# Kernel tuning notes

Hardware: AMD Instinct MI355X
Metric: run time of the kernel (lower is better)

The kernel has to match this reference:

```python
import jax, jax.numpy as jnp
import numpy as np

NUM_CODES = 4096
EMBED_DIM = 256
N_TOKENS = 65536
COMMITMENT_COST = 0.1


def setup_inputs() -> dict:
    key = jax.random.key(0)
    k1, k2 = jax.random.split(key)
    z_e = jax.random.normal(k1, (N_TOKENS, EMBED_DIM), dtype=jnp.float32)
    embeddings = jax.random.normal(k2, (NUM_CODES, EMBED_DIM), dtype=jnp.float32)
    return {"z_e": z_e, "embeddings": embeddings}


def reference(z_e, embeddings):
    # Squared Euclidean distances (argmin-equivalent to torch.cdist):
    # d2[n,k] = |z_n|^2 - 2 z_n.E_k + |E_k|^2
    z_sq = jnp.sum(z_e * z_e, axis=-1, keepdims=True)          # [N,1]
    e_sq = jnp.sum(embeddings * embeddings, axis=-1)            # [K]
    d2 = z_sq - 2.0 * (z_e @ embeddings.T) + e_sq[None, :]      # [N,K]
    indices = jnp.argmin(d2, axis=-1)                           # [N] int

    z_q = embeddings[indices]                                   # [N,D] gather

    # commitment loss: mse(detach(z_q), z_e)
    diff = jax.lax.stop_gradient(z_q) - z_e
    commitment_loss = COMMITMENT_COST * jnp.mean(diff * diff)

    # straight-through estimator
    z_q_st = z_e + jax.lax.stop_gradient(z_q - z_e)

    # perplexity from code usage histogram (avoids materializing one-hot)
    counts = jnp.zeros((NUM_CODES,), dtype=jnp.float32).at[indices].add(1.0)
    avg_probs = counts / z_e.shape[0]
    perplexity = jnp.exp(-jnp.sum(avg_probs * jnp.log(avg_probs + 1e-10)))

    return z_q_st, indices, commitment_loss, perplexity
```

## Files before the change

kernel.cpp:

```cpp
#include <hip/hip_runtime.h>

#define N_TOKENS   65536
#define NUM_CODES  4096
#define EMBED_DIM  256

#define IDX_OFF  ((size_t)N_TOKENS * EMBED_DIM)
#define LOSS_OFF (IDX_OFF + N_TOKENS)

#define DELTA 0.2f
#define UCAP  16384
#define RT    8

typedef _Float16 half8 __attribute__((ext_vector_type(8)));
typedef float    f32x4 __attribute__((ext_vector_type(4)));
typedef unsigned long long u64;

__device__ __forceinline__ void gl_lds16(const void* g, void* l) {
    __builtin_amdgcn_global_load_lds(
        (const __attribute__((address_space(1))) unsigned int*)g,
        (__attribute__((address_space(3))) unsigned int*)l, 16, 0, 0);
}

__global__ void k_convE(const float* __restrict__ E, _Float16* __restrict__ Eh) {
    int gid = blockIdx.x * 256 + threadIdx.x;
    int n  = gid >> 5;
    int kg = gid & 31;
    const float* src = E + (size_t)n * EMBED_DIM + kg * 8;
    float4 a = *(const float4*)src;
    float4 b = *(const float4*)(src + 4);
    int ct = n >> 4, l15 = n & 15, kc = kg >> 2, q = kg & 3;
    int lane = q * 16 + l15;
    half8 hv;
    hv[0]=(_Float16)a.x; hv[1]=(_Float16)a.y; hv[2]=(_Float16)a.z; hv[3]=(_Float16)a.w;
    hv[4]=(_Float16)b.x; hv[5]=(_Float16)b.y; hv[6]=(_Float16)b.z; hv[7]=(_Float16)b.w;
    *(half8*)(Eh + ((size_t)(ct * 8 + kc) * 64 + lane) * 8) = hv;
}

__global__ void k_esq(const float* __restrict__ E, float* __restrict__ esq) {
    int k = blockIdx.x;
    int l = threadIdx.x;
    float4 v = *(const float4*)(E + (size_t)k * EMBED_DIM + l * 4);
    float s = v.x * v.x + v.y * v.y + v.z * v.z + v.w * v.w;
    #pragma unroll
    for (int off = 32; off; off >>= 1) s += __shfl_down(s, off, 64);
    if (l == 0) esq[k] = s;
}

__global__ void k_transpose(const float* __restrict__ E, float* __restrict__ Et) {
    __shared__ float t[32][33];
    int tx = threadIdx.x & 31, ty = threadIdx.x >> 5;
    int c0 = blockIdx.x * 32, d0 = blockIdx.y * 32;
    #pragma unroll
    for (int i = 0; i < 4; ++i)
        t[ty + 8 * i][tx] = E[(size_t)(c0 + ty + 8 * i) * EMBED_DIM + d0 + tx];
    __syncthreads();
    #pragma unroll
    for (int i = 0; i < 4; ++i)
        Et[(size_t)(d0 + ty + 8 * i) * NUM_CODES + c0 + tx] = t[tx][ty + 8 * i];
}

__launch_bounds__(256, 2)
__global__ void k_argmin_mfma(const float* __restrict__ Z, const _Float16* __restrict__ Eh,
                              const float* __restrict__ esq, int* __restrict__ out_idx,
                              int* __restrict__ ulist, int* __restrict__ ucount) {
    __shared__ __align__(16) _Float16 Bs[16384];
    __shared__ float esq_s[NUM_CODES];

    const int tid  = threadIdx.x;
    const int lane = tid & 63;
    const int w    = tid >> 6;
    const int w0   = w >> 1;
    const int w1   = w & 1;
    const int l15  = lane & 15;
    const int q    = lane >> 4;
    const int tb   = blockIdx.x;

    for (int i = tid; i < NUM_CODES; i += 256) esq_s[i] = esq[i];

    half8 A[4][8];
    const float* Zb = Z + ((size_t)tb * 128 + w0 * 64) * EMBED_DIM;
    #pragma unroll
    for (int rt = 0; rt < 4; ++rt) {
        const float* Zr = Zb + (rt * 16 + l15) * EMBED_DIM + q * 8;
        #pragma unroll
        for (int kc = 0; kc < 8; ++kc) {
            float4 a = *(const float4*)(Zr + kc * 32);
            float4 b = *(const float4*)(Zr + kc * 32 + 4);
            half8 hv;
            hv[0]=(_Float16)a.x; hv[1]=(_Float16)a.y; hv[2]=(_Float16)a.z; hv[3]=(_Float16)a.w;
            hv[4]=(_Float16)b.x; hv[5]=(_Float16)b.y; hv[6]=(_Float16)b.z; hv[7]=(_Float16)b.w;
            A[rt][kc] = hv;
        }
    }

    float best[16], sec[16];
    int   bidx[16];
    #pragma unroll
    for (int k = 0; k < 16; ++k) { best[k] = 1e30f; sec[k] = 1e30f; bidx[k] = 0; }

    const int cb = w1 * 2;

    for (int it = 0; it < NUM_CODES / 64; ++it) {
        __syncthreads();
        const _Float16* src = Eh + (size_t)it * 16384 + (w * 8) * 512 + lane * 8;
        #pragma unroll
        for (int s = 0; s < 8; ++s)
            gl_lds16(src + s * 512, Bs + (w * 8 + s) * 512);
        __syncthreads();

        f32x4 acc[4][2];
        #pragma unroll
        for (int rt = 0; rt < 4; ++rt) { acc[rt][0] = (f32x4)0.0f; acc[rt][1] = (f32x4)0.0f; }

        #pragma unroll
        for (int kc = 0; kc < 8; ++kc) {
            half8 bf0 = *(const half8*)(Bs + ((cb + 0) * 8 + kc) * 512 + lane * 8);
            half8 bf1 = *(const half8*)(Bs + ((cb + 1) * 8 + kc) * 512 + lane * 8);
            #pragma unroll
            for (int rt = 0; rt < 4; ++rt) {
                acc[rt][0] = __builtin_amdgcn_mfma_f32_16x16x32_f16(A[rt][kc], bf0, acc[rt][0], 0, 0, 0);
                acc[rt][1] = __builtin_amdgcn_mfma_f32_16x16x32_f16(A[rt][kc], bf1, acc[rt][1], 0, 0, 0);
            }
        }

        int code0 = it * 64 + cb * 16 + l15;
        #pragma unroll
        for (int c = 0; c < 2; ++c) {
            float e  = esq_s[code0 + c * 16];
            int code = code0 + c * 16;
            #pragma unroll
            for (int rt = 0; rt < 4; ++rt)
                #pragma unroll
                for (int r = 0; r < 4; ++r) {
                    float v = fmaf(-2.0f, acc[rt][c][r], e);
                    int k = rt * 4 + r;
                    float ob = best[k];
                    bool t = v < ob;
                    best[k] = t ? v : ob;
                    sec[k]  = fminf(sec[k], t ? ob : v);
                    bidx[k] = t ? code : bidx[k];
                }
        }
    }

    #pragma unroll
    for (int m = 1; m <= 8; m <<= 1) {
        #pragma unroll
        for (int k = 0; k < 16; ++k) {
            float ob = __shfl_xor(best[k], m, 64);
            float os = __shfl_xor(sec[k],  m, 64);
            int   oi = __shfl_xor(bidx[k], m, 64);
            float ns = fminf(fminf(sec[k], os), fmaxf(best[k], ob));
            bool t = (ob < best[k]) || (ob == best[k] && oi < bidx[k]);
            best[k] = t ? ob : best[k];
            bidx[k] = t ? oi : bidx[k];
            sec[k]  = ns;
        }
    }

    __syncthreads();
    float* mb = (float*)Bs;
    float* ms = mb + 256;
    int*   mi = (int*)(mb + 512);
    if (l15 == 0) {
        #pragma unroll
        for (int k = 0; k < 16; ++k) {
            int row = w0 * 64 + (k >> 2) * 16 + q * 4 + (k & 3);
            mb[row * 2 + w1] = best[k];
            ms[row * 2 + w1] = sec[k];
            mi[row * 2 + w1] = bidx[k];
        }
    }
    __syncthreads();
    if (tid < 128) {
        float b0 = mb[tid * 2], b1 = mb[tid * 2 + 1];
        float s0 = ms[tid * 2], s1 = ms[tid * 2 + 1];
        int   i0 = mi[tid * 2], i1 = mi[tid * 2 + 1];
        bool t = (b1 < b0) || (b1 == b0 && i1 < i0);
        float bb = t ? b1 : b0;
        int   ii = t ? i1 : i0;
        float ss = fminf(fminf(s0, s1), fmaxf(b0, b1));
        int token = tb * 128 + tid;
        out_idx[token] = ii;
        if (ss - bb < DELTA) {
            int p = atomicAdd(ucount, 1);
            if (p < UCAP) ulist[p] = token;
        }
    }
}

__launch_bounds__(256)
__global__ void k_refine(const float* __restrict__ Z, const float* __restrict__ Et,
                         const float* __restrict__ esq, const int* __restrict__ ulist,
                         const int* __restrict__ ucount, u64* __restrict__ umin) {
    int cnt = *ucount; if (cnt > UCAP) cnt = UCAP;
    const int g   = blockIdx.x >> 2;
    const int qtr = blockIdx.x & 3;
    if (g * RT >= cnt) return;

    __shared__ float zs[RT][256];
    const int tid  = threadIdx.x;
    const int lane = tid & 63;

    #pragma unroll
    for (int t = 0; t < RT; ++t) {
        int u = g * RT + t;
        int tok = ulist[(u < cnt) ? u : g * RT];
        zs[t][tid] = Z[(size_t)tok * EMBED_DIM + tid];
    }
    __syncthreads();

    const int c0 = qtr * 1024 + tid * 4;
    f32x4 acc[RT];
    #pragma unroll
    for (int t = 0; t < RT; ++t) acc[t] = (f32x4)0.0f;

    for (int d4 = 0; d4 < 64; ++d4) {
        f32x4 e0 = *(const f32x4*)(Et + (size_t)(d4 * 4 + 0) * NUM_CODES + c0);
        f32x4 e1 = *(const f32x4*)(Et + (size_t)(d4 * 4 + 1) * NUM_CODES + c0);
        f32x4 e2 = *(const f32x4*)(Et + (size_t)(d4 * 4 + 2) * NUM_CODES + c0);
        f32x4 e3 = *(const f32x4*)(Et + (size_t)(d4 * 4 + 3) * NUM_CODES + c0);
        #pragma unroll
        for (int t = 0; t < RT; ++t) {
            f32x4 z4 = *(const f32x4*)&zs[t][d4 * 4];
            acc[t] += z4.x * e0;
            acc[t] += z4.y * e1;
            acc[t] += z4.z * e2;
            acc[t] += z4.w * e3;
        }
    }

    f32x4 eq = *(const f32x4*)(esq + c0);
    #pragma unroll
    for (int t = 0; t < RT; ++t) {
        u64 p = ~0ull;
        #pragma unroll
        for (int r = 0; r < 4; ++r) {
            float v = fmaf(-2.0f, acc[t][r], eq[r]) + 4096.0f;
            u64 cand = ((u64)__float_as_uint(v) << 32) | (unsigned)(c0 + r);
            p = cand < p ? cand : p;
        }
        #pragma unroll
        for (int m = 1; m <= 32; m <<= 1) {
            u64 o = __shfl_xor(p, m, 64);
            p = o < p ? o : p;
        }
        int u = g * RT + t;
        if (lane == 0 && u < cnt) atomicMin(umin + u, p);
    }
}

__global__ void k_rwrite(const int* __restrict__ ulist, const int* __restrict__ ucount,
                         const u64* __restrict__ umin, int* __restrict__ out_idx) {
    int cnt = *ucount; if (cnt > UCAP) cnt = UCAP;
    int u = blockIdx.x * 256 + threadIdx.x;
    if (u < cnt) out_idx[ulist[u]] = (int)(umin[u] & 0xFFFFFFFFu);
}

__global__ void k_gather(const float* __restrict__ Z, const float* __restrict__ E,
                         float* __restrict__ out,
                         float* __restrict__ loss_parts, unsigned* __restrict__ hist) {
    int wave = threadIdx.x >> 6, lane = threadIdx.x & 63;
    int token = blockIdx.x * 4 + wave;
    int* idxi = (int*)(out + IDX_OFF);
    int k = idxi[token];
    float4 z = *(const float4*)(Z + (size_t)token * EMBED_DIM + lane * 4);
    float4 qv = *(const float4*)(E + (size_t)k * EMBED_DIM + lane * 4);
    *(float4*)(out + (size_t)token * EMBED_DIM + lane * 4) = qv;
    float dx = qv.x - z.x, dy = qv.y - z.y, dz = qv.z - z.z, dw = qv.w - z.w;
    float s = dx * dx + dy * dy + dz * dz + dw * dw;
    #pragma unroll
    for (int off = 32; off; off >>= 1) s += __shfl_down(s, off, 64);
    if (lane == 0) {
        atomicAdd(loss_parts + (blockIdx.x & 1023), s);
        atomicAdd(hist + k, 1u);
        out[IDX_OFF + token] = (float)k;
    }
}

__global__ void k_final(const float* __restrict__ loss_parts,
                        const unsigned* __restrict__ hist, float* __restrict__ out) {
    __shared__ float red[256];
    int t = threadIdx.x;
    float s = 0.0f;
    for (int i = t; i < 1024; i += 256) s += loss_parts[i];
    red[t] = s;
    __syncthreads();
    #pragma unroll
    for (int off = 128; off; off >>= 1) {
        if (t < off) red[t] += red[t + off];
        __syncthreads();
    }
    float loss = 0.1f * red[0] / (float)(N_TOKENS * EMBED_DIM);

    float h = 0.0f;
    for (int i = t; i < NUM_CODES; i += 256) {
        float p = (float)hist[i] / (float)N_TOKENS;
        h += p * logf(p + 1e-10f);
    }
    __syncthreads();
    red[t] = h;
    __syncthreads();
    #pragma unroll
    for (int off = 128; off; off >>= 1) {
        if (t < off) red[t] += red[t + off];
        __syncthreads();
    }
    if (t == 0) {
        out[LOSS_OFF]     = loss;
        out[LOSS_OFF + 1] = expf(-red[0]);
    }
}

extern "C" void kernel_launch(void* const* d_in, const int* in_sizes, int n_in,
                              void* d_out, int out_size, void* d_ws, size_t ws_size,
                              hipStream_t stream) {
    const float* Z = (const float*)d_in[0];
    const float* E = (const float*)d_in[1];
    float* out = (float*)d_out;
    char*  ob  = (char*)d_out;
    char*  ws  = (char*)d_ws;

    _Float16* Eh   = (_Float16*)(ob + 50331648);
    float*    Et   = (float*)(ob + 54525952);
    u64*      umin = (u64*)(ob + 58720256);
    int*      idx  = (int*)(out + IDX_OFF);

    float*    esq        = (float*)ws;
    int*      ulist      = (int*)(ws + 16384);
    int*      ucount     = (int*)(ws + 81920);
    float*    loss_parts = (float*)(ws + 81984);
    unsigned* hist       = (unsigned*)(ws + 86080);

    hipMemsetAsync(ws + 81920, 0, 64 + 4096 + 16384, stream);
    hipMemsetAsync(umin, 0xFF, (size_t)UCAP * 8, stream);

    k_convE      <<<(NUM_CODES * 32) / 256, 256, 0, stream>>>(E, Eh);
    k_esq        <<<NUM_CODES, 64, 0, stream>>>(E, esq);
    k_transpose  <<<dim3(NUM_CODES / 32, EMBED_DIM / 32), 256, 0, stream>>>(E, Et);
    k_argmin_mfma<<<N_TOKENS / 128, 256, 0, stream>>>(Z, Eh, esq, idx, ulist, ucount);
    k_refine     <<<4 * (UCAP / RT), 256, 0, stream>>>(Z, Et, esq, ulist, ucount, umin);
    k_rwrite     <<<UCAP / 256, 256, 0, stream>>>(ulist, ucount, umin, idx);
    k_gather     <<<N_TOKENS / 4, 256, 0, stream>>>(Z, E, out, loss_parts, hist);
    k_final      <<<1, 256, 0, stream>>>(loss_parts, hist, out);
}
```

Baseline: 342.8 us.

## Double-buffer codebook LDS tiles and pair-reduce distances before the running argmin

The shared codebook tile becomes two buffers, so the async global-to-LDS copy of the next 64-code tile is issued before the MFMA work on the current tile. This hides load latency behind compute and cuts the barriers per tile from two to one. The argmin update now compares the two candidate codes per row with each other first, then merges the winner into the running best and second-best, which saves a compare chain per element. The trade-off is double the LDS for the tile, which at two blocks per CU leaves very little headroom and may hurt occupancy.

New measurement: 354.0 us. +3.3%, slower.

```diff
diff --git a/kernel.cpp b/kernel.cpp
--- a/kernel.cpp
+++ b/kernel.cpp
@@ -63,7 +63,7 @@
 __global__ void k_argmin_mfma(const float* __restrict__ Z, const _Float16* __restrict__ Eh,
                               const float* __restrict__ esq, int* __restrict__ out_idx,
                               int* __restrict__ ulist, int* __restrict__ ucount) {
-    __shared__ __align__(16) _Float16 Bs[16384];
+    __shared__ __align__(16) _Float16 Bs[2][16384];
     __shared__ float esq_s[NUM_CODES];
 
     const int tid  = threadIdx.x;
@@ -74,6 +74,16 @@
     const int l15  = lane & 15;
     const int q    = lane >> 4;
     const int tb   = blockIdx.x;
+    const int cb   = w1 * 2;
+
+#define STAGE(itn, nb) do {                                                        \
+        const _Float16* _src = Eh + (size_t)(itn) * 16384 + (w * 8) * 512 + lane * 8; \
+        _Pragma("unroll")                                                          \
+        for (int s = 0; s < 8; ++s)                                                \
+            gl_lds16(_src + s * 512, &Bs[nb][(w * 8 + s) * 512]);                  \
+    } while (0)
+
+    STAGE(0, 0);
 
     for (int i = tid; i < NUM_CODES; i += 256) esq_s[i] = esq[i];
 
@@ -98,50 +108,56 @@
     #pragma unroll
     for (int k = 0; k < 16; ++k) { best[k] = 1e30f; sec[k] = 1e30f; bidx[k] = 0; }
 
-    const int cb = w1 * 2;
-
-    for (int it = 0; it < NUM_CODES / 64; ++it) {
+    __syncthreads();
+
+#define COMPUTE(itv, nb) do {                                                      \
+        f32x4 acc[4][2];                                                           \
+        _Pragma("unroll")                                                          \
+        for (int rt = 0; rt < 4; ++rt) { acc[rt][0] = (f32x4)0.0f; acc[rt][1] = (f32x4)0.0f; } \
+        _Pragma("unroll")                                                          \
+        for (int kc = 0; kc < 8; ++kc) {                                           \
+            half8 bf0 = *(const half8*)(&Bs[nb][((cb + 0) * 8 + kc) * 512 + lane * 8]); \
+            half8 bf1 = *(const half8*)(&Bs[nb][((cb + 1) * 8 + kc) * 512 + lane * 8]); \
+            _Pragma("unroll")                                                      \
+            for (int rt = 0; rt < 4; ++rt) {                                       \
+                acc[rt][0] = __builtin_amdgcn_mfma_f32_16x16x32_f16(A[rt][kc], bf0, acc[rt][0], 0, 0, 0); \
+                acc[rt][1] = __builtin_amdgcn_mfma_f32_16x16x32_f16(A[rt][kc], bf1, acc[rt][1], 0, 0, 0); \
+            }                                                                      \
+        }                                                                          \
+        int code0 = (itv) * 64 + cb * 16 + l15;                                    \
+        int code1 = code0 + 16;                                                    \
+        float e0 = esq_s[code0];                                                   \
+        float e1 = esq_s[code1];                                                   \
+        _Pragma("unroll")                                                          \
+        for (int rt = 0; rt < 4; ++rt)                                             \
+            _Pragma("unroll")                                                      \
+            for (int r = 0; r < 4; ++r) {                                          \
+                int k = rt * 4 + r;                                                \
+                float v0 = fmaf(-2.0f, acc[rt][0][r], e0);                         \
+                float v1 = fmaf(-2.0f, acc[rt][1][r], e1);                         \
+                bool pw  = v1 < v0;                                                \
+                float wv = pw ? v1 : v0;                         \
+                float lv = pw ? v0 : v1;                         \
+                int   wi = pw ? code1 : code0;                                     \
+                float ob = best[k];                                                \
+                bool t = wv < ob;                                                  \
+                sec[k]  = fminf(fminf(fmaxf(ob, wv), lv), sec[k]);                 \
+                best[k] = t ? wv : ob;                                             \
+                bidx[k] = t ? wi : bidx[k];                                        \
+            }                                                                      \
+    } while (0)
+
+    for (int it = 0; it < NUM_CODES / 64; it += 2) {
+        STAGE(it + 1, 1);
+        COMPUTE(it, 0);
         __syncthreads();
-        const _Float16* src = Eh + (size_t)it * 16384 + (w * 8) * 512 + lane * 8;
-        #pragma unroll
-        for (int s = 0; s < 8; ++s)
-            gl_lds16(src + s * 512, Bs + (w * 8 + s) * 512);
+        if (it + 2 < NUM_CODES / 64) STAGE(it + 2, 0);
+        COMPUTE(it + 1, 1);
         __syncthreads();
-
-        f32x4 acc[4][2];
-        #pragma unroll
-        for (int rt = 0; rt < 4; ++rt) { acc[rt][0] = (f32x4)0.0f; acc[rt][1] = (f32x4)0.0f; }
-
-        #pragma unroll
-        for (int kc = 0; kc < 8; ++kc) {
-            half8 bf0 = *(const half8*)(Bs + ((cb + 0) * 8 + kc) * 512 + lane * 8);
-            half8 bf1 = *(const half8*)(Bs + ((cb + 1) * 8 + kc) * 512 + lane * 8);
-            #pragma unroll
-            for (int rt = 0; rt < 4; ++rt) {
-                acc[rt][0] = __builtin_amdgcn_mfma_f32_16x16x32_f16(A[rt][kc], bf0, acc[rt][0], 0, 0, 0);
-                acc[rt][1] = __builtin_amdgcn_mfma_f32_16x16x32_f16(A[rt][kc], bf1, acc[rt][1], 0, 0, 0);
-            }
-        }
-
-        int code0 = it * 64 + cb * 16 + l15;
-        #pragma unroll
-        for (int c = 0; c < 2; ++c) {
-            float e  = esq_s[code0 + c * 16];
-            int code = code0 + c * 16;
-            #pragma unroll
-            for (int rt = 0; rt < 4; ++rt)
-                #pragma unroll
-                for (int r = 0; r < 4; ++r) {
-                    float v = fmaf(-2.0f, acc[rt][c][r], e);
-                    int k = rt * 4 + r;
-                    float ob = best[k];
-                    bool t = v < ob;
-                    best[k] = t ? v : ob;
-                    sec[k]  = fminf(sec[k], t ? ob : v);
-                    bidx[k] = t ? code : bidx[k];
-                }
-        }
-    }
+    }
+
+#undef STAGE
+#undef COMPUTE
 
     #pragma unroll
     for (int m = 1; m <= 8; m <<= 1) {
```

## Stage Z tile in LDS and stream codebook fragments directly from global

Applied to the files above, without the earlier changes.

Z fragments now sit in LDS, loaded once per block, instead of registers. The codebook tiles are read straight from global memory (via L2/cache) instead of being staged into LDS with barriers each iteration. This removes the two per-iteration syncthreads and frees many VGPRs, but adds LDS reads of A per MFMA and uncoalesced-reuse global loads of B per wave. The min/second-min update is also restructured to first compare the two candidate codes pairwise, which cuts compare/select work.

New measurement: 388.6 us. 1.13x slower.

```diff
diff --git a/kernel.cpp b/kernel.cpp
--- a/kernel.cpp
+++ b/kernel.cpp
@@ -14,12 +14,6 @@
 typedef _Float16 half8 __attribute__((ext_vector_type(8)));
 typedef float    f32x4 __attribute__((ext_vector_type(4)));
 typedef unsigned long long u64;
-
-__device__ __forceinline__ void gl_lds16(const void* g, void* l) {
-    __builtin_amdgcn_global_load_lds(
-        (const __attribute__((address_space(1))) unsigned int*)g,
-        (__attribute__((address_space(3))) unsigned int*)l, 16, 0, 0);
-}
 
 __global__ void k_convE(const float* __restrict__ E, _Float16* __restrict__ Eh) {
     int gid = blockIdx.x * 256 + threadIdx.x;
@@ -63,7 +57,7 @@
 __global__ void k_argmin_mfma(const float* __restrict__ Z, const _Float16* __restrict__ Eh,
                               const float* __restrict__ esq, int* __restrict__ out_idx,
                               int* __restrict__ ulist, int* __restrict__ ucount) {
-    __shared__ __align__(16) _Float16 Bs[16384];
+    __shared__ __align__(16) _Float16 As[32768];
     __shared__ float esq_s[NUM_CODES];
 
     const int tid  = threadIdx.x;
@@ -72,24 +66,30 @@
     const int w0   = w >> 1;
     const int w1   = w & 1;
     const int l15  = lane & 15;
-    const int q    = lane >> 4;
     const int tb   = blockIdx.x;
+    const int cb   = w1 * 2;
 
     for (int i = tid; i < NUM_CODES; i += 256) esq_s[i] = esq[i];
 
-    half8 A[4][8];
-    const float* Zb = Z + ((size_t)tb * 128 + w0 * 64) * EMBED_DIM;
-    #pragma unroll
-    for (int rt = 0; rt < 4; ++rt) {
-        const float* Zr = Zb + (rt * 16 + l15) * EMBED_DIM + q * 8;
-        #pragma unroll
-        for (int kc = 0; kc < 8; ++kc) {
-            float4 a = *(const float4*)(Zr + kc * 32);
-            float4 b = *(const float4*)(Zr + kc * 32 + 4);
+    {
+        const float* Zb = Z + (size_t)tb * 128 * EMBED_DIM;
+        for (int i = tid; i < 4096; i += 256) {
+            int h  = i >> 11;
+            int fr = (i >> 6) & 31;
+            int ln = i & 63;
+            int rt = fr >> 3;
+            int kc = fr & 7;
+            int q  = ln >> 4;
+            int fl = ln & 15;
+            int n  = h * 64 + rt * 16 + fl;
+            int kg = kc * 4 + q;
+            const float* src = Zb + (size_t)n * EMBED_DIM + kg * 8;
+            float4 a = *(const float4*)src;
+            float4 b = *(const float4*)(src + 4);
             half8 hv;
             hv[0]=(_Float16)a.x; hv[1]=(_Float16)a.y; hv[2]=(_Float16)a.z; hv[3]=(_Float16)a.w;
             hv[4]=(_Float16)b.x; hv[5]=(_Float16)b.y; hv[6]=(_Float16)b.z; hv[7]=(_Float16)b.w;
-            A[rt][kc] = hv;
+            *(half8*)(As + (size_t)i * 8) = hv;
         }
     }
 
@@ -98,15 +98,12 @@
     #pragma unroll
     for (int k = 0; k < 16; ++k) { best[k] = 1e30f; sec[k] = 1e30f; bidx[k] = 0; }
 
-    const int cb = w1 * 2;
+    __syncthreads();
+
+    const int abase = w0 * 16384;
 
     for (int it = 0; it < NUM_CODES / 64; ++it) {
-        __syncthreads();
-        const _Float16* src = Eh + (size_t)it * 16384 + (w * 8) * 512 + lane * 8;
-        #pragma unroll
-        for (int s = 0; s < 8; ++s)
-            gl_lds16(src + s * 512, Bs + (w * 8 + s) * 512);
-        __syncthreads();
+        const _Float16* Bb = Eh + (size_t)it * 16384;
 
         f32x4 acc[4][2];
         #pragma unroll
@@ -114,33 +111,37 @@
 
         #pragma unroll
         for (int kc = 0; kc < 8; ++kc) {
-            half8 bf0 = *(const half8*)(Bs + ((cb + 0) * 8 + kc) * 512 + lane * 8);
-            half8 bf1 = *(const half8*)(Bs + ((cb + 1) * 8 + kc) * 512 + lane * 8);
+            half8 bf0 = *(const half8*)(Bb + ((cb + 0) * 8 + kc) * 512 + lane * 8);
+            half8 bf1 = *(const half8*)(Bb + ((cb + 1) * 8 + kc) * 512 + lane * 8);
             #pragma unroll
             for (int rt = 0; rt < 4; ++rt) {
-                acc[rt][0] = __builtin_amdgcn_mfma_f32_16x16x32_f16(A[rt][kc], bf0, acc[rt][0], 0, 0, 0);
-                acc[rt][1] = __builtin_amdgcn_mfma_f32_16x16x32_f16(A[rt][kc], bf1, acc[rt][1], 0, 0, 0);
+                half8 av = *(const half8*)(As + abase + ((rt * 8 + kc) * 64 + lane) * 8);
+                acc[rt][0] = __builtin_amdgcn_mfma_f32_16x16x32_f16(av, bf0, acc[rt][0], 0, 0, 0);
+                acc[rt][1] = __builtin_amdgcn_mfma_f32_16x16x32_f16(av, bf1, acc[rt][1], 0, 0, 0);
             }
         }
 
         int code0 = it * 64 + cb * 16 + l15;
-        #pragma unroll
-        for (int c = 0; c < 2; ++c) {
-            float e  = esq_s[code0 + c * 16];
-            int code = code0 + c * 16;
+        int code1 = code0 + 16;
+        float e0 = esq_s[code0];
+        float e1 = esq_s[code1];
+        #pragma unroll
+        for (int rt = 0; rt < 4; ++rt)
             #pragma unroll
-            for (int rt = 0; rt < 4; ++rt)
-                #pragma unroll
-                for (int r = 0; r < 4; ++r) {
-                    float v = fmaf(-2.0f, acc[rt][c][r], e);
-                    int k = rt * 4 + r;
-                    float ob = best[k];
-                    bool t = v < ob;
-                    best[k] = t ? v : ob;
-                    sec[k]  = fminf(sec[k], t ? ob : v);
-                    bidx[k] = t ? code : bidx[k];
-                }
-        }
+            for (int r = 0; r < 4; ++r) {
+                int k = rt * 4 + r;
+                float v0 = fmaf(-2.0f, acc[rt][0][r], e0);
+                float v1 = fmaf(-2.0f, acc[rt][1][r], e1);
+                bool pw  = v1 < v0;
+                float wv = pw ? v1 : v0;
+                float lv = pw ? v0 : v1;
+                int   wi = pw ? code1 : code0;
+                float ob = best[k];
+                bool t = wv < ob;
+                sec[k]  = fminf(fminf(fmaxf(ob, wv), lv), sec[k]);
+                best[k] = t ? wv : ob;
+                bidx[k] = t ? wi : bidx[k];
+            }
     }
 
     #pragma unroll
@@ -159,9 +160,10 @@
     }
 
     __syncthreads();
-    float* mb = (float*)Bs;
+    float* mb = (float*)As;
     float* ms = mb + 256;
     int*   mi = (int*)(mb + 512);
+    const int q = lane >> 4;
     if (l15 == 0) {
         #pragma unroll
         for (int k = 0; k < 16; ++k) {
```

## Double-buffer codebook tiles and give each wave all 64 codes per tile

Applied to the files above, without the earlier changes.

The codebook tile load moves to a two-stage LDS double buffer, prefetched two iterations ahead with explicit vmcnt waits and barriers, so global-to-LDS copies overlap the MFMA work. Work is redistributed so each wave owns 32 tokens and all 64 codes of a tile. This removes the cross-wave LDS merge at the end and halves the A-fragment registers. It adds s_setprio around the MFMA block and a tree-style min over four candidates per row, at the cost of twice the LDS (which may limit occupancy) and hand-written waitcnt logic that must match the load count.

Result: slower. 350.0 us (+2.1%).

```diff
diff --git a/kernel.cpp b/kernel.cpp
--- a/kernel.cpp
+++ b/kernel.cpp
@@ -59,28 +59,37 @@
         Et[(size_t)(d0 + ty + 8 * i) * NUM_CODES + c0 + tx] = t[tx][ty + 8 * i];
 }
 
-__launch_bounds__(256, 2)
-__global__ void k_argmin_mfma(const float* __restrict__ Z, const _Float16* __restrict__ Eh,
-                              const float* __restrict__ esq, int* __restrict__ out_idx,
-                              int* __restrict__ ulist, int* __restrict__ ucount) {
-    __shared__ __align__(16) _Float16 Bs[16384];
+__global__ __launch_bounds__(256) __attribute__((amdgpu_waves_per_eu(2, 2)))
+void k_argmin_mfma(const float* __restrict__ Z, const _Float16* __restrict__ Eh,
+                   const float* __restrict__ esq, int* __restrict__ out_idx,
+                   int* __restrict__ ulist, int* __restrict__ ucount) {
+    __shared__ __align__(16) _Float16 Bs[2][16384];
     __shared__ float esq_s[NUM_CODES];
 
     const int tid  = threadIdx.x;
     const int lane = tid & 63;
     const int w    = tid >> 6;
-    const int w0   = w >> 1;
-    const int w1   = w & 1;
     const int l15  = lane & 15;
     const int q    = lane >> 4;
     const int tb   = blockIdx.x;
 
+#define STAGE(itn, bb) do {                                                        \
+        const _Float16* _src = Eh + ((size_t)(itn) << 14) + (w * 8) * 512 + lane * 8; \
+        _Float16* _dst = &Bs[bb][(w * 8) * 512];                                   \
+        _Pragma("unroll")                                                          \
+        for (int s = 0; s < 8; ++s)                                                \
+            gl_lds16(_src + s * 512, _dst + s * 512);                              \
+    } while (0)
+
+    STAGE(0, 0);
+    STAGE(1, 1);
+
     for (int i = tid; i < NUM_CODES; i += 256) esq_s[i] = esq[i];
 
-    half8 A[4][8];
-    const float* Zb = Z + ((size_t)tb * 128 + w0 * 64) * EMBED_DIM;
-    #pragma unroll
-    for (int rt = 0; rt < 4; ++rt) {
+    half8 A[2][8];
+    const float* Zb = Z + ((size_t)tb * 128 + w * 32) * EMBED_DIM;
+    #pragma unroll
+    for (int rt = 0; rt < 2; ++rt) {
         const float* Zr = Zb + (rt * 16 + l15) * EMBED_DIM + q * 8;
         #pragma unroll
         for (int kc = 0; kc < 8; ++kc) {
@@ -93,60 +102,81 @@
         }
     }
 
-    float best[16], sec[16];
-    int   bidx[16];
-    #pragma unroll
-    for (int k = 0; k < 16; ++k) { best[k] = 1e30f; sec[k] = 1e30f; bidx[k] = 0; }
-
-    const int cb = w1 * 2;
+    float best[8], sec[8];
+    int   bidx[8];
+    #pragma unroll
+    for (int k = 0; k < 8; ++k) { best[k] = 1e30f; sec[k] = 1e30f; bidx[k] = 0; }
+
+    __syncthreads();
 
     for (int it = 0; it < NUM_CODES / 64; ++it) {
-        __syncthreads();
-        const _Float16* src = Eh + (size_t)it * 16384 + (w * 8) * 512 + lane * 8;
-        #pragma unroll
-        for (int s = 0; s < 8; ++s)
-            gl_lds16(src + s * 512, Bs + (w * 8 + s) * 512);
-        __syncthreads();
-
-        f32x4 acc[4][2];
-        #pragma unroll
-        for (int rt = 0; rt < 4; ++rt) { acc[rt][0] = (f32x4)0.0f; acc[rt][1] = (f32x4)0.0f; }
-
+        const int b = it & 1;
+
+        if (it == NUM_CODES / 64 - 1) asm volatile("s_waitcnt vmcnt(0)" ::: "memory");
+        else                          asm volatile("s_waitcnt vmcnt(8)" ::: "memory");
+        asm volatile("s_barrier" ::: "memory");
+
+        f32x4 acc[2][4];
+        #pragma unroll
+        for (int rt = 0; rt < 2; ++rt)
+            #pragma unroll
+            for (int ct = 0; ct < 4; ++ct) acc[rt][ct] = (f32x4)0.0f;
+
+        __builtin_amdgcn_s_setprio(1);
         #pragma unroll
         for (int kc = 0; kc < 8; ++kc) {
-            half8 bf0 = *(const half8*)(Bs + ((cb + 0) * 8 + kc) * 512 + lane * 8);
-            half8 bf1 = *(const half8*)(Bs + ((cb + 1) * 8 + kc) * 512 + lane * 8);
+            half8 bf[4];
             #pragma unroll
-            for (int rt = 0; rt < 4; ++rt) {
-                acc[rt][0] = __builtin_amdgcn_mfma_f32_16x16x32_f16(A[rt][kc], bf0, acc[rt][0], 0, 0, 0);
-                acc[rt][1] = __builtin_amdgcn_mfma_f32_16x16x32_f16(A[rt][kc], bf1, acc[rt][1], 0, 0, 0);
+            for (int ct = 0; ct < 4; ++ct)
+                bf[ct] = *(const half8*)(&Bs[b][(ct * 8 + kc) * 512 + lane * 8]);
+            #pragma unroll
+            for (int rt = 0; rt < 2; ++rt)
+                #pragma unroll
+                for (int ct = 0; ct < 4; ++ct)
+                    acc[rt][ct] = __builtin_amdgcn_mfma_f32_16x16x32_f16(A[rt][kc], bf[ct], acc[rt][ct], 0, 0, 0);
+        }
+        __builtin_amdgcn_s_setprio(0);
+
+        const int code_base = it * 64 + l15;
+        float e0 = esq_s[code_base];
+        float e1 = esq_s[code_base + 16];
+        float e2 = esq_s[code_base + 32];
+        float e3 = esq_s[code_base + 48];
+        #pragma unroll
+        for (int rt = 0; rt < 2; ++rt)
+            #pragma unroll
+            for (int r = 0; r < 4; ++r) {
+                int k = rt * 4 + r;
+                float v0 = fmaf(-2.0f, acc[rt][0][r], e0);
+                float v1 = fmaf(-2.0f, acc[rt][1][r], e1);
+                float v2 = fmaf(-2.0f, acc[rt][2][r], e2);
+                float v3 = fmaf(-2.0f, acc[rt][3][r], e3);
+                bool t01 = v1 < v0;
+                float w01 = t01 ? v1 : v0, l01 = t01 ? v0 : v1;
+                int   i01 = code_base + (t01 ? 16 : 0);
+                bool t23 = v3 < v2;
+                float w23 = t23 ? v3 : v2, l23 = t23 ? v2 : v3;
+                int   i23 = code_base + 32 + (t23 ? 16 : 0);
+                bool tf = w23 < w01;
+                float wv = tf ? w23 : w01;
+                int   wi = tf ? i23 : i01;
+                float rsec = fminf(fminf(fmaxf(w01, w23), l01), l23);
+                float ob = best[k];
+                bool tb_ = wv < ob;
+                sec[k]  = fminf(fminf(sec[k], rsec), fmaxf(ob, wv));
+                best[k] = tb_ ? wv : ob;
+                bidx[k] = tb_ ? wi : bidx[k];
             }
-        }
-
-        int code0 = it * 64 + cb * 16 + l15;
-        #pragma unroll
-        for (int c = 0; c < 2; ++c) {
-            float e  = esq_s[code0 + c * 16];
-            int code = code0 + c * 16;
-            #pragma unroll
-            for (int rt = 0; rt < 4; ++rt)
-                #pragma unroll
-                for (int r = 0; r < 4; ++r) {
-                    float v = fmaf(-2.0f, acc[rt][c][r], e);
-                    int k = rt * 4 + r;
-                    float ob = best[k];
-                    bool t = v < ob;
-                    best[k] = t ? v : ob;
-                    sec[k]  = fminf(sec[k], t ? ob : v);
-                    bidx[k] = t ? code : bidx[k];
-                }
-        }
-    }
+
+        asm volatile("s_barrier" ::: "memory");
+        if (it + 2 < NUM_CODES / 64) STAGE(it + 2, b);
+    }
+#undef STAGE
 
     #pragma unroll
     for (int m = 1; m <= 8; m <<= 1) {
         #pragma unroll
-        for (int k = 0; k < 16; ++k) {
+        for (int k = 0; k < 8; ++k) {
             float ob = __shfl_xor(best[k], m, 64);
             float os = __shfl_xor(sec[k],  m, 64);
             int   oi = __shfl_xor(bidx[k], m, 64);
@@ -158,33 +188,16 @@
         }
     }
 
-    __syncthreads();
-    float* mb = (float*)Bs;
-    float* ms = mb + 256;
-    int*   mi = (int*)(mb + 512);
     if (l15 == 0) {
         #pragma unroll
-        for (int k = 0; k < 16; ++k) {
-            int row = w0 * 64 + (k >> 2) * 16 + q * 4 + (k & 3);
-            mb[row * 2 + w1] = best[k];
-            ms[row * 2 + w1] = sec[k];
-            mi[row * 2 + w1] = bidx[k];
-        }
-    }
-    __syncthreads();
-    if (tid < 128) {
-        float b0 = mb[tid * 2], b1 = mb[tid * 2 + 1];
-        float s0 = ms[tid * 2], s1 = ms[tid * 2 + 1];
-        int   i0 = mi[tid * 2], i1 = mi[tid * 2 + 1];
-        bool t = (b1 < b0) || (b1 == b0 && i1 < i0);
-        float bb = t ? b1 : b0;
-        int   ii = t ? i1 : i0;
-        float ss = fminf(fminf(s0, s1), fmaxf(b0, b1));
-        int token = tb * 128 + tid;
-        out_idx[token] = ii;
-        if (ss - bb < DELTA) {
-            int p = atomicAdd(ucount, 1);
-            if (p < UCAP) ulist[p] = token;
+        for (int k = 0; k < 8; ++k) {
+            int row   = w * 32 + (k >> 2) * 16 + q * 4 + (k & 3);
+            int token = tb * 128 + row;
+            out_idx[token] = bidx[k];
+            if (sec[k] - best[k] < DELTA) {
+                int p = atomicAdd(ucount, 1);
+                if (p < UCAP) ulist[p] = token;
+            }
         }
     }
 }
```
